# Kernel optimization log

Hardware: AMD Instinct MI355X
Metric: run time of the kernel (lower is better)

The kernel has to match this reference:

```python
import jax, jax.numpy as jnp
import numpy as np

N_NODES = 100000
N_EDGES = 1600000
N_GRAPHS = 512


def _graph_conv(x, W, b, src, dst, n_nodes):
    """DGL GraphConv, norm='both': D_in^-1/2 (A (D_out^-1/2 x)) W + b.
    Weight is applied on the smaller-dim side (same math, less memory)."""
    ones = jnp.ones(src.shape[0], dtype=x.dtype)
    deg_out = jnp.clip(jax.ops.segment_sum(ones, src, num_segments=n_nodes), 1.0)
    deg_in = jnp.clip(jax.ops.segment_sum(ones, dst, num_segments=n_nodes), 1.0)
    h = x * (deg_out ** -0.5)[:, None]
    if W.shape[0] > W.shape[1]:  # reduce feature dim before the SpMM
        h = h @ W
        h = jax.ops.segment_sum(h[src], dst, num_segments=n_nodes)
    else:
        h = jax.ops.segment_sum(h[src], dst, num_segments=n_nodes)
        h = h @ W
    return h * (deg_in ** -0.5)[:, None] + b


def setup_inputs() -> dict:
    key = jax.random.key(0)
    ks = jax.random.split(key, 16)
    x = jax.random.normal(ks[0], (N_NODES, 128), dtype=jnp.float32)
    src = jax.random.randint(ks[1], (N_EDGES,), 0, N_NODES, dtype=jnp.int32)
    dst = jax.random.randint(ks[2], (N_EDGES,), 0, N_NODES, dtype=jnp.int32)
    graph_ids = jnp.sort(jax.random.randint(ks[3], (N_NODES,), 0, N_GRAPHS, dtype=jnp.int32))
    s = 0.05
    return {
        "x": x, "src": src, "dst": dst, "graph_ids": graph_ids,
        "W1": jax.random.normal(ks[4], (128, 256), jnp.float32) * s,
        "b1": jnp.zeros((256,), jnp.float32),
        "W2": jax.random.normal(ks[5], (256, 64), jnp.float32) * s,
        "b2": jnp.zeros((64,), jnp.float32),
        "Wc1": jax.random.normal(ks[6], (64, 18), jnp.float32) * s,
        "bc1": jnp.zeros((18,), jnp.float32),
        "Wc2": jax.random.normal(ks[7], (18, 12), jnp.float32) * s,
        "bc2": jnp.zeros((12,), jnp.float32),
        "Wc3": jax.random.normal(ks[8], (12, 6), jnp.float32) * s,
        "bc3": jnp.zeros((6,), jnp.float32),
        "Wc4": jax.random.normal(ks[9], (6, 2), jnp.float32) * s,
        "bc4": jnp.zeros((2,), jnp.float32),
    }


def reference(x, src, dst, graph_ids, W1, b1, W2, b2, Wc1, bc1, Wc2, bc2, Wc3, bc3, Wc4, bc4):
    n = x.shape[0]
    h = jax.nn.relu(_graph_conv(x, W1, b1, src, dst, n))
    h = jax.nn.relu(_graph_conv(h, W2, b2, src, dst, n))
    # dgl.mean_nodes: per-graph mean over nodes
    sums = jax.ops.segment_sum(h, graph_ids, num_segments=N_GRAPHS)
    cnts = jnp.clip(jax.ops.segment_sum(jnp.ones(n, h.dtype), graph_ids, num_segments=N_GRAPHS), 1.0)
    hg = sums / cnts[:, None]
    # classifier: 4 stacked Linear layers, no activations (faithful to source)
    hg = hg @ Wc1 + bc1
    hg = hg @ Wc2 + bc2
    hg = hg @ Wc3 + bc3
    return hg @ Wc4 + bc4
```

## Files before the change

kernel.cpp:

```cpp
#include <hip/hip_runtime.h>
#include <cstdint>
#include <cstddef>

#define NGRAPHS 512

static inline size_t align_up(size_t x, size_t a){ return (x + a - 1) & ~(a - 1); }

__device__ __forceinline__ unsigned short f2bf(float f){
  unsigned int u = __float_as_uint(f);
  u += 0x7FFFu + ((u >> 16) & 1u);
  return (unsigned short)(u >> 16);
}
__device__ __forceinline__ float bflo(unsigned int u){ return __uint_as_float(u << 16); }
__device__ __forceinline__ float bfhi(unsigned int u){ return __uint_as_float(u & 0xffff0000u); }
__device__ __forceinline__ unsigned int pack2(float a, float b){
  return (unsigned)f2bf(a) | ((unsigned)f2bf(b) << 16);
}

typedef __attribute__((ext_vector_type(8))) short bf16x8;
typedef __attribute__((ext_vector_type(4))) float f32x4;

__global__ __launch_bounds__(256) void k_partcount(const int* __restrict__ src, const int* __restrict__ dst,
                                                   int* __restrict__ cntS, int* __restrict__ cntD, int n_edges, int NBLK,
                                                   const float* __restrict__ W1, unsigned short* __restrict__ Wt1,
                                                   const float* __restrict__ W2, unsigned short* __restrict__ Wt2,
                                                   const int* __restrict__ gids, int* __restrict__ gb, int n_nodes){
  __shared__ int cs[256], cd[256];
  if (blockIdx.x >= NBLK){
    long long u = (long long)(blockIdx.x - NBLK) * 256 + threadIdx.x;
    if (u < 128 * 256){
      int k = (int)(u / 256), n = (int)(u % 256);
      Wt1[(size_t)n * 128 + k] = f2bf(W1[u]);
      return;
    }
    u -= 128 * 256;
    if (u < 256 * 64){
      int k = (int)(u / 64), n = (int)(u % 64);
      Wt2[(size_t)n * 256 + k] = f2bf(W2[u]);
      return;
    }
    u -= 256 * 64;
    if (u < n_nodes){
      int i = (int)u;
      int g  = gids[i];
      int gp = (i > 0) ? gids[i - 1] : -1;
      for (int q = gp + 1; q <= g; ++q) gb[q] = i;
      if (i == n_nodes - 1)
        for (int q = g + 1; q <= NGRAPHS; ++q) gb[q] = n_nodes;
    }
    return;
  }
  int tid = threadIdx.x;
  cs[tid] = 0; cd[tid] = 0;
  __syncthreads();
  int e0 = blockIdx.x * 4096;
  int e1 = min(e0 + 4096, n_edges);
  for (int e = e0 + tid; e < e1; e += 256){
    atomicAdd(&cs[src[e] >> 9], 1);
    atomicAdd(&cd[dst[e] >> 9], 1);
  }
  __syncthreads();
  cntS[blockIdx.x * 256 + tid] = cs[tid];
  cntD[blockIdx.x * 256 + tid] = cd[tid];
}

__global__ __launch_bounds__(256) void k_colscan(int* __restrict__ cntS, int* __restrict__ cntD,
                                                 int* __restrict__ totS, int* __restrict__ totD,
                                                 int nblk, int NB){
  int col = blockIdx.x;
  int* cnt; int* tot; int k;
  if (col < NB){ cnt = cntS; tot = totS; k = col; }
  else         { cnt = cntD; tot = totD; k = col - NB; }
  __shared__ int tsum[256];
  int tid = threadIdx.x;
  int i0 = 2 * tid, i1 = 2 * tid + 1;
  int a = (i0 < nblk) ? cnt[i0 * 256 + k] : 0;
  int b = (i1 < nblk) ? cnt[i1 * 256 + k] : 0;
  int s = a + b;
  tsum[tid] = s;
  __syncthreads();
  for (int off = 1; off < 256; off <<= 1){
    int t = (tid >= off) ? tsum[tid - off] : 0;
    __syncthreads();
    tsum[tid] += t;
    __syncthreads();
  }
  int pre = tsum[tid] - s;
  if (i0 < nblk) cnt[i0 * 256 + k] = pre;
  if (i1 < nblk) cnt[i1 * 256 + k] = pre + a;
  if (tid == 255) tot[k] = tsum[255];
}

__global__ __launch_bounds__(256) void k_scatter_det(const int* __restrict__ src, const int* __restrict__ dst,
                                                     const int* __restrict__ cntS, const int* __restrict__ cntD,
                                                     const int* __restrict__ totS, const int* __restrict__ totD,
                                                     int* __restrict__ baseS, int* __restrict__ baseD,
                                                     int2* __restrict__ pairD, int* __restrict__ srcS,
                                                     int n_edges, int NB){
  __shared__ int s1[256], s2[256];
  __shared__ int gbS[256], gbD[256], lsS[256], lsD[256], lcS[256], lcD[256];
  __shared__ int2 ebuf[4096];
  __shared__ int sbuf[4096];
  int tid = threadIdx.x;
  int b = blockIdx.x;
  int v1 = (tid < NB) ? totS[tid] : 0;
  int v2 = (tid < NB) ? totD[tid] : 0;
  s1[tid] = v1; s2[tid] = v2;
  __syncthreads();
  for (int off = 1; off < 256; off <<= 1){
    int t1 = (tid >= off) ? s1[tid - off] : 0;
    int t2 = (tid >= off) ? s2[tid - off] : 0;
    __syncthreads();
    s1[tid] += t1; s2[tid] += t2;
    __syncthreads();
  }
  int bS = s1[tid] - v1, bD = s2[tid] - v2;
  if (b == 0 && tid < NB){ baseS[tid] = bS; baseD[tid] = bD; }
  gbS[tid] = bS + cntS[b * 256 + tid];
  gbD[tid] = bD + cntD[b * 256 + tid];
  __syncthreads();
  int e0 = b * 4096, e1 = min(e0 + 4096, n_edges);
  int ne = e1 - e0;
  s1[tid] = 0; s2[tid] = 0;
  __syncthreads();
  for (int e = e0 + tid; e < e1; e += 256){
    atomicAdd(&s1[src[e] >> 9], 1);
    atomicAdd(&s2[dst[e] >> 9], 1);
  }
  __syncthreads();
  int hv1 = s1[tid], hv2 = s2[tid];
  __syncthreads();
  s1[tid] = hv1; s2[tid] = hv2;
  __syncthreads();
  for (int off = 1; off < 256; off <<= 1){
    int t1 = (tid >= off) ? s1[tid - off] : 0;
    int t2 = (tid >= off) ? s2[tid - off] : 0;
    __syncthreads();
    s1[tid] += t1; s2[tid] += t2;
    __syncthreads();
  }
  lsS[tid] = s1[tid] - hv1; lcS[tid] = lsS[tid];
  lsD[tid] = s2[tid] - hv2; lcD[tid] = lsD[tid];
  __syncthreads();
  for (int e = e0 + tid; e < e1; e += 256){
    int s = src[e], d = dst[e];
    int lp = atomicAdd(&lcD[d >> 9], 1);
    ebuf[lp] = make_int2(s, d);
    int sp = atomicAdd(&lcS[s >> 9], 1);
    sbuf[sp] = s;
  }
  __syncthreads();
  for (int i = tid; i < ne; i += 256){
    int2 e = ebuf[i];
    int kd = e.y >> 9;
    pairD[gbD[kd] + i - lsD[kd]] = e;
    int sv = sbuf[i];
    int ks = sv >> 9;
    srcS[gbS[ks] + i - lsS[ks]] = sv;
  }
}

__global__ __launch_bounds__(256) void k_bucket_build(const int2* __restrict__ pairD, const int* __restrict__ baseD,
                                                      const int* __restrict__ srcS, const int* __restrict__ baseS,
                                                      int* __restrict__ offs, float* __restrict__ din_s,
                                                      float* __restrict__ dout_s, int* __restrict__ csr_src,
                                                      const float* __restrict__ x, unsigned int* __restrict__ xb,
                                                      int NB, int n, int n_edges){
  __shared__ int cd[512], cs[512], cur[512];
  __shared__ float sds[512];
  __shared__ int tsum[256];
  int b = blockIdx.x, node0 = b << 9, tid = threadIdx.x;
  int nn = min(512, n - node0);
  for (int i = tid; i < 512; i += 256){ cd[i] = 0; cs[i] = 0; }
  __syncthreads();
  int jd0 = baseD[b], jd1 = (b + 1 < NB) ? baseD[b + 1] : n_edges;
  for (int j = jd0 + tid; j < jd1; j += 256) atomicAdd(&cd[pairD[j].y - node0], 1);
  int js0 = baseS[b], js1 = (b + 1 < NB) ? baseS[b + 1] : n_edges;
  for (int j = js0 + tid; j < js1; j += 256) atomicAdd(&cs[srcS[j] - node0], 1);
  __syncthreads();
  int a0 = cd[2 * tid], a1 = cd[2 * tid + 1];
  int s = a0 + a1;
  tsum[tid] = s;
  __syncthreads();
  for (int off = 1; off < 256; off <<= 1){
    int t = (tid >= off) ? tsum[tid - off] : 0;
    __syncthreads();
    tsum[tid] += t;
    __syncthreads();
  }
  int pre = tsum[tid] - s + jd0;
  cur[2 * tid]     = pre;
  cur[2 * tid + 1] = pre + a0;
  __syncthreads();
  for (int i = tid; i < nn; i += 256){
    offs[node0 + i]   = cur[i];
    din_s[node0 + i]  = 1.0f / sqrtf((float)max(cd[i], 1));
    float od = 1.0f / sqrtf((float)max(cs[i], 1));
    dout_s[node0 + i] = od;
    sds[i] = od;
  }
  if (b == NB - 1 && tid == 0) offs[n] = n_edges;
  __syncthreads();
  for (int j = jd0 + tid; j < jd1; j += 256){
    int2 e = pairD[j];
    int p = atomicAdd(&cur[e.y - node0], 1);
    csr_src[p] = e.x;
  }
  const float4* x4 = (const float4*)x;
  int tot = nn * 32;
  for (int i = tid; i < tot; i += 256){
    float4 v = x4[(size_t)node0 * 32 + i];
    float sc = sds[i >> 5];
    size_t o2 = ((size_t)node0 * 32 + i) * 2;
    xb[o2 + 0] = pack2(v.x * sc, v.y * sc);
    xb[o2 + 1] = pack2(v.z * sc, v.w * sc);
  }
}

__global__ __launch_bounds__(256) void k_spmm1(const unsigned int* __restrict__ xb,
    const int* __restrict__ offs, const int* __restrict__ csr_src,
    unsigned int* __restrict__ aggb, int n_nodes){
  int node = __builtin_amdgcn_readfirstlane((int)((blockIdx.x * 256u + threadIdx.x) >> 6));
  if (node >= n_nodes) return;
  int lane = threadIdx.x & 63;
  int j0 = offs[node], j1 = offs[node + 1];
  float ax = 0.f, ay = 0.f;
  int j = j0;
  for (; j + 4 <= j1; j += 4){
    int s0 = csr_src[j + 0];
    int s1 = csr_src[j + 1];
    int s2 = csr_src[j + 2];
    int s3 = csr_src[j + 3];
    unsigned v0 = xb[(size_t)s0 * 64 + lane];
    unsigned v1 = xb[(size_t)s1 * 64 + lane];
    unsigned v2 = xb[(size_t)s2 * 64 + lane];
    unsigned v3 = xb[(size_t)s3 * 64 + lane];
    ax += bflo(v0) + bflo(v1) + bflo(v2) + bflo(v3);
    ay += bfhi(v0) + bfhi(v1) + bfhi(v2) + bfhi(v3);
  }
  for (; j < j1; ++j){
    unsigned v = xb[(size_t)csr_src[j] * 64 + lane];
    ax += bflo(v);
    ay += bfhi(v);
  }
  aggb[(size_t)node * 64 + lane] = pack2(ax, ay);
}

__global__ __launch_bounds__(256) void k_gemm1(const unsigned short* __restrict__ A,
    const unsigned short* __restrict__ Bt, unsigned short* __restrict__ C,
    int M, const float* __restrict__ din, const float* __restrict__ dout,
    const float* __restrict__ bias){
  constexpr int LDA = 136;
  __shared__ __align__(16) unsigned short As[128 * LDA];
  __shared__ __align__(16) unsigned short Bs[64 * LDA];
  int tid = threadIdx.x;
  int bm0 = blockIdx.x * 128;
  int wid = tid >> 6, lane = tid & 63;
  int wm = wid * 32;
  int quad = lane >> 4, l16 = lane & 15;

  uint4 areg[8];
#pragma unroll
  for (int it = 0; it < 8; ++it){
    int i = tid + it * 256;
    int m = i >> 4, c = i & 15;
    int gr = bm0 + m;
    areg[it] = (gr < M) ? *(const uint4*)(A + (size_t)gr * 128 + c * 8) : make_uint4(0u, 0u, 0u, 0u);
  }
  uint4 breg[4];
#pragma unroll
  for (int it = 0; it < 4; ++it){
    int i = tid + it * 256;
    int n = i >> 4, c = i & 15;
    breg[it] = *(const uint4*)(Bt + (size_t)n * 128 + c * 8);
  }
#pragma unroll
  for (int it = 0; it < 8; ++it){
    int i = tid + it * 256;
    int m = i >> 4, c = i & 15;
    *(uint4*)&As[m * LDA + c * 8] = areg[it];
  }
#pragma unroll
  for (int it = 0; it < 4; ++it){
    int i = tid + it * 256;
    int n = i >> 4, c = i & 15;
    *(uint4*)&Bs[n * LDA + c * 8] = breg[it];
  }
  float rsv[2][4], rs2v[2][4];
#pragma unroll
  for (int t = 0; t < 2; ++t)
#pragma unroll
    for (int r = 0; r < 4; ++r){
      int gr = bm0 + wm + t * 16 + quad * 4 + r;
      rsv[t][r]  = (gr < M) ? din[gr]  : 0.f;
      rs2v[t][r] = (gr < M) ? dout[gr] : 0.f;
    }
  __syncthreads();

  for (int nt = 0; nt < 4; ++nt){
    if (nt < 3){
#pragma unroll
      for (int it = 0; it < 4; ++it){
        int i = tid + it * 256;
        int n = i >> 4, c = i & 15;
        breg[it] = *(const uint4*)(Bt + (size_t)((nt + 1) * 64 + n) * 128 + c * 8);
      }
    }
    f32x4 acc[2][4];
#pragma unroll
    for (int t = 0; t < 2; ++t)
#pragma unroll
      for (int u = 0; u < 4; ++u) acc[t][u] = f32x4{0.f, 0.f, 0.f, 0.f};
#pragma unroll
    for (int ks = 0; ks < 4; ++ks){
      bf16x8 af[2], bfr[4];
#pragma unroll
      for (int t = 0; t < 2; ++t)
        af[t] = *(const bf16x8*)&As[(wm + t * 16 + l16) * LDA + ks * 32 + quad * 8];
#pragma unroll
      for (int u = 0; u < 4; ++u)
        bfr[u] = *(const bf16x8*)&Bs[(u * 16 + l16) * LDA + ks * 32 + quad * 8];
#pragma unroll
      for (int t = 0; t < 2; ++t)
#pragma unroll
        for (int u = 0; u < 4; ++u)
          acc[t][u] = __builtin_amdgcn_mfma_f32_16x16x32_bf16(af[t], bfr[u], acc[t][u], 0, 0, 0);
    }
    float bv[4];
#pragma unroll
    for (int u = 0; u < 4; ++u) bv[u] = bias[nt * 64 + u * 16 + l16];
#pragma unroll
    for (int t = 0; t < 2; ++t){
#pragma unroll
      for (int r = 0; r < 4; ++r){
        int gr = bm0 + wm + t * 16 + quad * 4 + r;
        if (gr < M){
#pragma unroll
          for (int u = 0; u < 4; ++u){
            float cv = fmaxf(fmaf(acc[t][u][r], rsv[t][r], bv[u]), 0.f) * rs2v[t][r];
            C[(size_t)gr * 256 + nt * 64 + u * 16 + l16] = f2bf(cv);
          }
        }
      }
    }
    if (nt < 3){
      __syncthreads();
#pragma unroll
      for (int it = 0; it < 4; ++it){
        int i = tid + it * 256;
        int n = i >> 4, c = i & 15;
        *(uint4*)&Bs[n * LDA + c * 8] = breg[it];
      }
      __syncthreads();
    }
  }
}

#define SCHUNK 4
__global__ __launch_bounds__(256) void k_spmm2_fused(const unsigned short* __restrict__ t2,
    const int* __restrict__ offs, const int* __restrict__ csr_src,
    const float* __restrict__ din_s, const float* __restrict__ b2,
    const int* __restrict__ gb, float* __restrict__ sums){
  __shared__ float bs[64];
  int tid = threadIdx.x;
  int g = blockIdx.x & (NGRAPHS - 1);
  int chunk = blockIdx.x >> 9;
  int wW = __builtin_amdgcn_readfirstlane(chunk * 4 + (tid >> 6));
  int lane = tid & 63, half = lane >> 5, l = lane & 31;
  if (tid < 64) bs[tid] = 0.f;
  __syncthreads();
  int g0 = gb[g], g1 = gb[g + 1];
  const unsigned int* tp = (const unsigned int*)t2;
  float2 bb = ((const float2*)b2)[l];
  float gxs = 0.f, gys = 0.f;
  for (int node = g0 + wW; node < g1; node += 16){
    int j0 = offs[node], j1 = offs[node + 1];
    float ax = 0.f, ay = 0.f;
    int j = j0;
    for (; j + 2 <= j1; j += 2){
      int s0 = csr_src[j], s1 = csr_src[j + 1];
      int ss = half ? s1 : s0;
      unsigned v = tp[(size_t)ss * 32 + l];
      ax += bflo(v);
      ay += bfhi(v);
    }
    if (j < j1 && half == 0){
      unsigned v = tp[(size_t)csr_src[j] * 32 + l];
      ax += bflo(v);
      ay += bfhi(v);
    }
    ax += __shfl_xor(ax, 32);
    ay += __shfl_xor(ay, 32);
    float ds = din_s[node];
    gxs += fmaxf(fmaf(ax, ds, bb.x), 0.f);
    gys += fmaxf(fmaf(ay, ds, bb.y), 0.f);
  }
  if (half == 0){
    atomicAdd(&bs[2 * l], gxs);
    atomicAdd(&bs[2 * l + 1], gys);
  }
  __syncthreads();
  if (tid < 64) atomicAdd(&sums[(size_t)g * 64 + tid], bs[tid]);
}

template<bool C_BF16, bool EPI, bool EPI2>
__global__ __launch_bounds__(256) void gemm_mfma(
    const unsigned short* __restrict__ A, const unsigned short* __restrict__ Bt, void* __restrict__ Cp,
    int M, int N, int K,
    const float* __restrict__ rowScaleC, const float* __restrict__ rowScaleC2,
    const float* __restrict__ bias){
  constexpr int BM = 128, BN = 64, BK = 32, LDA = 40;
  __shared__ __align__(16) unsigned short As[2][BM * LDA];
  __shared__ __align__(16) unsigned short Bs[2][BN * LDA];
  int tid = threadIdx.x;
  int bm0 = blockIdx.x * BM;
  int bn0 = blockIdx.y * BN;
  int wid = tid >> 6, lane = tid & 63;
  int wm = (wid >> 1) * 64, wn = (wid & 1) * 32;
  int quad = lane >> 4, l16 = lane & 15;
  f32x4 acc[4][2];
#pragma unroll
  for (int t = 0; t < 4; ++t)
#pragma unroll
    for (int u = 0; u < 2; ++u) acc[t][u] = f32x4{0.f, 0.f, 0.f, 0.f};

  uint2 ar[4], br[2];
  auto preload = [&](int kk){
#pragma unroll
    for (int it = 0; it < 4; ++it){
      int i = tid + it * 256;
      int m = i >> 3, c = i & 7;
      int gr = bm0 + m;
      ar[it] = (gr < M) ? *(const uint2*)(A + (size_t)gr * K + kk + c * 4) : make_uint2(0u, 0u);
    }
#pragma unroll
    for (int it = 0; it < 2; ++it){
      int i = tid + it * 256;
      int n = i >> 3, c = i & 7;
      br[it] = *(const uint2*)(Bt + (size_t)(bn0 + n) * K + kk + c * 4);
    }
  };
  auto commit = [&](int buf){
#pragma unroll
    for (int it = 0; it < 4; ++it){
      int i = tid + it * 256;
      int m = i >> 3, c = i & 7;
      *(uint2*)&As[buf][m * LDA + c * 4] = ar[it];
    }
#pragma unroll
    for (int it = 0; it < 2; ++it){
      int i = tid + it * 256;
      int n = i >> 3, c = i & 7;
      *(uint2*)&Bs[buf][n * LDA + c * 4] = br[it];
    }
  };

  preload(0);
  commit(0);
  __syncthreads();
  int nk = K / BK;
  for (int kb = 0; kb < nk; ++kb){
    int cur = kb & 1;
    if (kb + 1 < nk) preload((kb + 1) * BK);
    bf16x8 af[4], bfr[2];
#pragma unroll
    for (int t = 0; t < 4; ++t)
      af[t] = *(const bf16x8*)&As[cur][(wm + t * 16 + l16) * LDA + quad * 8];
#pragma unroll
    for (int u = 0; u < 2; ++u)
      bfr[u] = *(const bf16x8*)&Bs[cur][(wn + u * 16 + l16) * LDA + quad * 8];
#pragma unroll
    for (int t = 0; t < 4; ++t)
#pragma unroll
      for (int u = 0; u < 2; ++u)
        acc[t][u] = __builtin_amdgcn_mfma_f32_16x16x32_bf16(af[t], bfr[u], acc[t][u], 0, 0, 0);
    if (kb + 1 < nk){
      commit(cur ^ 1);
      __syncthreads();
    }
  }
  float bv[2] = {0.f, 0.f};
  if constexpr (EPI){ bv[0] = bias[bn0 + wn + l16]; bv[1] = bias[bn0 + wn + 16 + l16]; }
#pragma unroll
  for (int t = 0; t < 4; ++t){
#pragma unroll
    for (int r = 0; r < 4; ++r){
      int gr = bm0 + wm + t * 16 + quad * 4 + r;
      if (gr < M){
        float rs = 1.f, rs2 = 1.f;
        if constexpr (EPI)  rs  = rowScaleC[gr];
        if constexpr (EPI2) rs2 = rowScaleC2[gr];
#pragma unroll
        for (int u = 0; u < 2; ++u){
          int gc = bn0 + wn + u * 16 + l16;
          float cv = acc[t][u][r];
          if constexpr (EPI)  cv = fmaxf(fmaf(cv, rs, bv[u]), 0.f);
          if constexpr (EPI2) cv *= rs2;
          if constexpr (C_BF16) ((unsigned short*)Cp)[(size_t)gr * N + gc] = f2bf(cv);
          else                  ((float*)Cp)[(size_t)gr * N + gc] = cv;
        }
      }
    }
  }
}

__global__ __launch_bounds__(256) void k_classifier(const float* __restrict__ sums, const int* __restrict__ gb,
    const float* __restrict__ Wc1, const float* __restrict__ bc1,
    const float* __restrict__ Wc2, const float* __restrict__ bc2,
    const float* __restrict__ Wc3, const float* __restrict__ bc3,
    const float* __restrict__ Wc4, const float* __restrict__ bc4,
    float* __restrict__ out){
  __shared__ float w1[64 * 18], w2[18 * 12], w3[12 * 6], w4[6 * 2];
  __shared__ float B1[18], B2[12], B3[6], B4[2];
  int tid = threadIdx.x;
  for (int i = tid; i < 64 * 18; i += 256) w1[i] = Wc1[i];
  for (int i = tid; i < 18 * 12; i += 256) w2[i] = Wc2[i];
  for (int i = tid; i < 12 * 6;  i += 256) w3[i] = Wc3[i];
  for (int i = tid; i < 6 * 2;   i += 256) w4[i] = Wc4[i];
  if (tid < 18) B1[tid] = bc1[tid];
  if (tid < 12) B2[tid] = bc2[tid];
  if (tid < 6)  B3[tid] = bc3[tid];
  if (tid < 2)  B4[tid] = bc4[tid];
  __syncthreads();
  int g = blockIdx.x * 256 + tid;
  float cnt = fmaxf((float)(gb[g + 1] - gb[g]), 1.0f);
  float h[64];
#pragma unroll
  for (int f = 0; f < 64; ++f) h[f] = sums[(size_t)g * 64 + f] / cnt;
  float t1[18];
#pragma unroll
  for (int j = 0; j < 18; ++j){
    float s = B1[j];
    for (int f = 0; f < 64; ++f) s = fmaf(h[f], w1[f * 18 + j], s);
    t1[j] = s;
  }
  float t2[12];
#pragma unroll
  for (int j = 0; j < 12; ++j){
    float s = B2[j];
    for (int f = 0; f < 18; ++f) s = fmaf(t1[f], w2[f * 12 + j], s);
    t2[j] = s;
  }
  float t3[6];
#pragma unroll
  for (int j = 0; j < 6; ++j){
    float s = B3[j];
    for (int f = 0; f < 12; ++f) s = fmaf(t2[f], w3[f * 6 + j], s);
    t3[j] = s;
  }
#pragma unroll
  for (int j = 0; j < 2; ++j){
    float s = B4[j];
    for (int f = 0; f < 6; ++f) s = fmaf(t3[f], w4[f * 2 + j], s);
    out[(size_t)g * 2 + j] = s;
  }
}

extern "C" void kernel_launch(void* const* d_in, const int* in_sizes, int n_in,
                              void* d_out, int out_size, void* d_ws, size_t ws_size,
                              hipStream_t stream){
  const float* x   = (const float*)d_in[0];
  const int*   src = (const int*)d_in[1];
  const int*   dst = (const int*)d_in[2];
  const int*   gid = (const int*)d_in[3];
  const float* W1  = (const float*)d_in[4];
  const float* b1  = (const float*)d_in[5];
  const float* W2  = (const float*)d_in[6];
  const float* b2  = (const float*)d_in[7];
  const float* Wc1 = (const float*)d_in[8];
  const float* bc1 = (const float*)d_in[9];
  const float* Wc2 = (const float*)d_in[10];
  const float* bc2 = (const float*)d_in[11];
  const float* Wc3 = (const float*)d_in[12];
  const float* bc3 = (const float*)d_in[13];
  const float* Wc4 = (const float*)d_in[14];
  const float* bc4 = (const float*)d_in[15];
  float* out = (float*)d_out;

  const int n_nodes = in_sizes[3];
  const int n_edges = in_sizes[1];
  const int F1 = 256, F2 = 64;
  const int NB   = (n_nodes + 511) >> 9;
  const int NBLK = (n_edges + 4095) / 4096;

  char* w = (char*)d_ws;
  size_t o = 0;
  auto alloc = [&](size_t bytes) -> char* {
    char* p = w + o;
    o = align_up(o + bytes, 256);
    return p;
  };
  float* sums      = (float*)alloc((size_t)NGRAPHS * F2 * 4);
  int*   gb        = (int*)  alloc((size_t)(NGRAPHS + 1) * 4);
  int*   cntS      = (int*)  alloc((size_t)NBLK * 256 * 4);
  int*   cntD      = (int*)  alloc((size_t)NBLK * 256 * 4);
  int*   totS      = (int*)  alloc((size_t)256 * 4);
  int*   totD      = (int*)  alloc((size_t)256 * 4);
  int*   baseS     = (int*)  alloc((size_t)256 * 4);
  int*   baseD     = (int*)  alloc((size_t)256 * 4);
  float* dout_s    = (float*)alloc((size_t)n_nodes * 4);
  float* din_s     = (float*)alloc((size_t)n_nodes * 4);
  int*   offs      = (int*)  alloc((size_t)(n_nodes + 1) * 4);
  int*   csr_src   = (int*)  alloc((size_t)n_edges * 4);
  unsigned short* Wt1 = (unsigned short*)alloc((size_t)256 * 128 * 2);
  unsigned short* Wt2 = (unsigned short*)alloc((size_t)64 * 256 * 2);
  unsigned int*   xb  = (unsigned int*)  alloc((size_t)n_nodes * 128 * 2);
  unsigned short* aggb= (unsigned short*)alloc((size_t)n_nodes * 128 * 2);
  unsigned short* h1b = (unsigned short*)alloc((size_t)n_nodes * F1 * 2);
  int2*  pairD = (int2*)aggb;
  int*   srcS  = (int*)((char*)aggb + (size_t)n_edges * 8);
  unsigned short* t2b = aggb;

  hipMemsetAsync(sums, 0, (size_t)NGRAPHS * F2 * 4, stream);

  {
    long long miscTotal = 128 * 256 + 256 * 64 + n_nodes;
    int miscBlocks = (int)((miscTotal + 255) / 256);
    k_partcount<<<NBLK + miscBlocks, 256, 0, stream>>>(src, dst, cntS, cntD, n_edges, NBLK,
                                                       W1, Wt1, W2, Wt2, gid, gb, n_nodes);
  }
  k_colscan     <<<2 * NB, 256, 0, stream>>>(cntS, cntD, totS, totD, NBLK, NB);
  k_scatter_det <<<NBLK, 256, 0, stream>>>(src, dst, cntS, cntD, totS, totD, baseS, baseD, pairD, srcS, n_edges, NB);
  k_bucket_build<<<NB, 256, 0, stream>>>(pairD, baseD, srcS, baseS, offs, din_s, dout_s, csr_src,
                                         x, xb, NB, n_nodes, n_edges);

  int gx = (n_nodes + 127) / 128;
  {
    long long threads = (long long)n_nodes * 64;
    k_spmm1<<<(int)((threads + 255) / 256), 256, 0, stream>>>(xb, offs, csr_src, (unsigned int*)aggb, n_nodes);
    k_gemm1<<<gx, 256, 0, stream>>>(aggb, Wt1, h1b, n_nodes, din_s, dout_s, b1);
  }
  {
    gemm_mfma<true, false, false><<<dim3(gx, 1), 256, 0, stream>>>(
        h1b, Wt2, t2b, n_nodes, F2, F1, nullptr, nullptr, nullptr);
    k_spmm2_fused<<<NGRAPHS * SCHUNK, 256, 0, stream>>>(t2b, offs, csr_src, din_s, b2, gb, sums);
  }
  k_classifier<<<NGRAPHS / 256, 256, 0, stream>>>(sums, gb, Wc1, bc1, Wc2, bc2, Wc3, bc3, Wc4, bc4, out);
}
```

Baseline: 376.1 us.

## Split bucket build into dst/src block halves and move x prescale to separate kernel

```diff
diff --git a/kernel.cpp b/kernel.cpp
--- a/kernel.cpp
+++ b/kernel.cpp
@@ -143,11 +143,11 @@
   lsD[tid] = s2[tid] - hv2; lcD[tid] = lsD[tid];
   __syncthreads();
   for (int e = e0 + tid; e < e1; e += 256){
-    int s = src[e], d = dst[e];
+    int sv = src[e], d = dst[e];
     int lp = atomicAdd(&lcD[d >> 9], 1);
-    ebuf[lp] = make_int2(s, d);
-    int sp = atomicAdd(&lcS[s >> 9], 1);
-    sbuf[sp] = s;
+    ebuf[lp] = make_int2(sv, d);
+    int sp = atomicAdd(&lcS[sv >> 9], 1);
+    sbuf[sp] = sv;
   }
   __syncthreads();
   for (int i = tid; i < ne; i += 256){
@@ -164,57 +164,64 @@
                                                       const int* __restrict__ srcS, const int* __restrict__ baseS,
                                                       int* __restrict__ offs, float* __restrict__ din_s,
                                                       float* __restrict__ dout_s, int* __restrict__ csr_src,
-                                                      const float* __restrict__ x, unsigned int* __restrict__ xb,
                                                       int NB, int n, int n_edges){
-  __shared__ int cd[512], cs[512], cur[512];
-  __shared__ float sds[512];
+  __shared__ int cnt[512], cur[512];
   __shared__ int tsum[256];
-  int b = blockIdx.x, node0 = b << 9, tid = threadIdx.x;
+  int tid = threadIdx.x;
+  int bb = blockIdx.x;
+  bool dstSide = bb < NB;
+  int b = dstSide ? bb : bb - NB;
+  int node0 = b << 9;
   int nn = min(512, n - node0);
-  for (int i = tid; i < 512; i += 256){ cd[i] = 0; cs[i] = 0; }
-  __syncthreads();
-  int jd0 = baseD[b], jd1 = (b + 1 < NB) ? baseD[b + 1] : n_edges;
-  for (int j = jd0 + tid; j < jd1; j += 256) atomicAdd(&cd[pairD[j].y - node0], 1);
-  int js0 = baseS[b], js1 = (b + 1 < NB) ? baseS[b + 1] : n_edges;
-  for (int j = js0 + tid; j < js1; j += 256) atomicAdd(&cs[srcS[j] - node0], 1);
-  __syncthreads();
-  int a0 = cd[2 * tid], a1 = cd[2 * tid + 1];
-  int s = a0 + a1;
-  tsum[tid] = s;
-  __syncthreads();
-  for (int off = 1; off < 256; off <<= 1){
-    int t = (tid >= off) ? tsum[tid - off] : 0;
-    __syncthreads();
-    tsum[tid] += t;
-    __syncthreads();
-  }
-  int pre = tsum[tid] - s + jd0;
-  cur[2 * tid]     = pre;
-  cur[2 * tid + 1] = pre + a0;
-  __syncthreads();
-  for (int i = tid; i < nn; i += 256){
-    offs[node0 + i]   = cur[i];
-    din_s[node0 + i]  = 1.0f / sqrtf((float)max(cd[i], 1));
-    float od = 1.0f / sqrtf((float)max(cs[i], 1));
-    dout_s[node0 + i] = od;
-    sds[i] = od;
-  }
-  if (b == NB - 1 && tid == 0) offs[n] = n_edges;
-  __syncthreads();
-  for (int j = jd0 + tid; j < jd1; j += 256){
-    int2 e = pairD[j];
-    int p = atomicAdd(&cur[e.y - node0], 1);
-    csr_src[p] = e.x;
-  }
-  const float4* x4 = (const float4*)x;
-  int tot = nn * 32;
-  for (int i = tid; i < tot; i += 256){
-    float4 v = x4[(size_t)node0 * 32 + i];
-    float sc = sds[i >> 5];
-    size_t o2 = ((size_t)node0 * 32 + i) * 2;
-    xb[o2 + 0] = pack2(v.x * sc, v.y * sc);
-    xb[o2 + 1] = pack2(v.z * sc, v.w * sc);
-  }
+  for (int i = tid; i < 512; i += 256) cnt[i] = 0;
+  __syncthreads();
+  if (dstSide){
+    int jd0 = baseD[b], jd1 = (b + 1 < NB) ? baseD[b + 1] : n_edges;
+    for (int j = jd0 + tid; j < jd1; j += 256) atomicAdd(&cnt[pairD[j].y - node0], 1);
+    __syncthreads();
+    int a0 = cnt[2 * tid], a1 = cnt[2 * tid + 1];
+    int s = a0 + a1;
+    tsum[tid] = s;
+    __syncthreads();
+    for (int off = 1; off < 256; off <<= 1){
+      int t = (tid >= off) ? tsum[tid - off] : 0;
+      __syncthreads();
+      tsum[tid] += t;
+      __syncthreads();
+    }
+    int pre = tsum[tid] - s + jd0;
+    cur[2 * tid]     = pre;
+    cur[2 * tid + 1] = pre + a0;
+    __syncthreads();
+    for (int i = tid; i < nn; i += 256){
+      offs[node0 + i]  = cur[i];
+      din_s[node0 + i] = 1.0f / sqrtf((float)max(cnt[i], 1));
+    }
+    if (b == NB - 1 && tid == 0) offs[n] = n_edges;
+    __syncthreads();
+    for (int j = jd0 + tid; j < jd1; j += 256){
+      int2 e = pairD[j];
+      int p = atomicAdd(&cur[e.y - node0], 1);
+      csr_src[p] = e.x;
+    }
+  } else {
+    int js0 = baseS[b], js1 = (b + 1 < NB) ? baseS[b + 1] : n_edges;
+    for (int j = js0 + tid; j < js1; j += 256) atomicAdd(&cnt[srcS[j] - node0], 1);
+    __syncthreads();
+    for (int i = tid; i < nn; i += 256)
+      dout_s[node0 + i] = 1.0f / sqrtf((float)max(cnt[i], 1));
+  }
+}
+
+__global__ __launch_bounds__(256) void k_prep2(const float* __restrict__ x,
+                                               const float* __restrict__ dout_s,
+                                               unsigned int* __restrict__ xb, long long total4){
+  long long t = (long long)blockIdx.x * 256 + threadIdx.x;
+  if (t >= total4) return;
+  float4 v = ((const float4*)x)[t];
+  float s = dout_s[t >> 5];
+  xb[t * 2 + 0] = pack2(v.x * s, v.y * s);
+  xb[t * 2 + 1] = pack2(v.z * s, v.w * s);
 }
 
 __global__ __launch_bounds__(256) void k_spmm1(const unsigned int* __restrict__ xb,
@@ -621,8 +628,13 @@
   }
   k_colscan     <<<2 * NB, 256, 0, stream>>>(cntS, cntD, totS, totD, NBLK, NB);
   k_scatter_det <<<NBLK, 256, 0, stream>>>(src, dst, cntS, cntD, totS, totD, baseS, baseD, pairD, srcS, n_edges, NB);
-  k_bucket_build<<<NB, 256, 0, stream>>>(pairD, baseD, srcS, baseS, offs, din_s, dout_s, csr_src,
-                                         x, xb, NB, n_nodes, n_edges);
+  k_bucket_build<<<2 * NB, 256, 0, stream>>>(pairD, baseD, srcS, baseS, offs, din_s, dout_s, csr_src,
+                                             NB, n_nodes, n_edges);
+
+  {
+    long long total4 = (long long)n_nodes * 32;
+    k_prep2<<<(int)((total4 + 255) / 256), 256, 0, stream>>>(x, dout_s, xb, total4);
+  }
 
   int gx = (n_nodes + 127) / 128;
   {
```

After: 357.0 us. 5.1% less time.
